# Kernel optimization log

Hardware: AMD Instinct MI355X
Metric: run time of the kernel (lower is better)

Reference implementation:

```python
import jax, jax.numpy as jnp
import numpy as np

N = 8192
E = 131072
D_IN = 128
D_OUT = 128
EPS = 1e-5


def setup_inputs() -> dict:
    key = jax.random.key(0)
    k1, k2, k3, k4 = jax.random.split(key, 4)
    x = jax.random.normal(k1, (N, D_IN), dtype=jnp.float32)
    edge_index = jax.random.randint(k2, (2, E), 0, N, dtype=jnp.int64)
    weight = jax.random.normal(k3, (D_IN, D_OUT), dtype=jnp.float32)
    bias = jax.random.normal(k4, (D_OUT,), dtype=jnp.float32)
    return {"x": x, "edge_index": edge_index, "weight": weight, "bias": bias}


def reference(x, edge_index, weight, bias):
    n = x.shape[0]
    row, col = edge_index[0], edge_index[1]
    # dense adjacency build, exactly as the torch module does
    adj = jnp.zeros((n, n), dtype=x.dtype).at[row, col].set(1.0)
    adj = jnp.maximum(adj, adj.T)                      # symmetrize
    adj = adj + jnp.eye(n, dtype=x.dtype)              # self-loops (added, may yield 2 on diag)
    d_inv_sqrt = 1.0 / jnp.sqrt(adj.sum(axis=1) + EPS)  # [N]
    # D^{-1/2} A D^{-1/2} via broadcasting (same math as diag matmuls)
    norm_adj = d_inv_sqrt[:, None] * adj * d_inv_sqrt[None, :]
    out = norm_adj @ x            # [N, D_IN] aggregation
    out = out @ weight + bias     # [N, D_OUT]
    return out
```

## Files before the change

### kernel.cpp

```cpp
#include <hip/hip_runtime.h>
#include <stdint.h>

#define N_NODES 8192
#define NE      131072
#define DCH     128
#define WPR     256
#define MAXC    128
#define EPS     1e-5f

__global__ __launch_bounds__(256) void build_gemm_kernel(
    const void*  __restrict__ ei_raw,
    const float* __restrict__ X,
    const float* __restrict__ W,
    uint32_t* __restrict__ bm,
    int*      __restrict__ deg,
    float*    __restrict__ z)
{
    int t = threadIdx.x;
    if (blockIdx.x < 512) {
        int lane = t & 63;
        const long long* p64 = (const long long*)ei_raw;
        const int*       p32 = (const int*)ei_raw;
        bool is64 = __all((unsigned long long)p64[lane] < (unsigned long long)N_NODES);
        int e = blockIdx.x * 256 + t;
        int r, c;
        if (is64) { r = (int)p64[e]; c = (int)p64[NE + e]; }
        else      { r = p32[e];      c = p32[NE + e]; }
        uint32_t mc = 1u << (c & 31), mr = 1u << (r & 31);
        uint32_t o1 = atomicOr(&bm[r * WPR + (c >> 5)], mc);
        if (!(o1 & mc)) atomicAdd(&deg[r], 1);
        uint32_t o2 = atomicOr(&bm[c * WPR + (r >> 5)], mr);
        if (!(o2 & mr)) atomicAdd(&deg[c], 1);
    } else {
        __shared__ float sA[64][132];
        int bx = blockIdx.x - 512;
        int row0 = (bx >> 1) * 64;
        int col0 = (bx & 1) * 64;
        {
            int k4 = t & 31;
            int r  = t >> 5;
            #pragma unroll
            for (int p = 0; p < 8; ++p) {
                float4 v = *(const float4*)&X[(size_t)(row0 + r + p * 8) * DCH + k4 * 4];
                *(float4*)&sA[r + p * 8][k4 * 4] = v;
            }
        }
        __syncthreads();
        int tx = t & 15, ty = t >> 4;
        int cg = col0 + tx * 4;
        int r0 = ty * 4;
        float acc[4][4] = {};
        #pragma unroll 4
        for (int k = 0; k < DCH; ++k) {
            float4 w = *(const float4*)&W[(size_t)k * DCH + cg];
            float a0 = sA[r0 + 0][k];
            float a1 = sA[r0 + 1][k];
            float a2 = sA[r0 + 2][k];
            float a3 = sA[r0 + 3][k];
            acc[0][0] += a0 * w.x; acc[0][1] += a0 * w.y; acc[0][2] += a0 * w.z; acc[0][3] += a0 * w.w;
            acc[1][0] += a1 * w.x; acc[1][1] += a1 * w.y; acc[1][2] += a1 * w.z; acc[1][3] += a1 * w.w;
            acc[2][0] += a2 * w.x; acc[2][1] += a2 * w.y; acc[2][2] += a2 * w.z; acc[2][3] += a2 * w.w;
            acc[3][0] += a3 * w.x; acc[3][1] += a3 * w.y; acc[3][2] += a3 * w.z; acc[3][3] += a3 * w.w;
        }
        #pragma unroll
        for (int i = 0; i < 4; ++i) {
            float4 o;
            o.x = acc[i][0]; o.y = acc[i][1]; o.z = acc[i][2]; o.w = acc[i][3];
            *(float4*)&z[(size_t)(row0 + r0 + i) * DCH + cg] = o;
        }
    }
}

__global__ __launch_bounds__(256) void aggregate_kernel(
    const uint4* __restrict__ bm4,
    const int*   __restrict__ deg,
    const float* __restrict__ z,
    const float* __restrict__ bias,
    float*       __restrict__ out)
{
    __shared__ uint16_t slist[4][MAXC];
    int w    = threadIdx.x >> 6;
    int lane = threadIdx.x & 63;
    int node = blockIdx.x * 4 + w;

    uint4 b = bm4[(size_t)node * 64 + lane];
    int c = __popc(b.x) + __popc(b.y) + __popc(b.z) + __popc(b.w);
    int pre = c;
    #pragma unroll
    for (int d = 1; d < 64; d <<= 1) {
        int v = __shfl_up(pre, d);
        if (lane >= d) pre += v;
    }
    int total = __shfl(pre, 63);
    int excl  = pre - c;

    {
        uint32_t wd[4] = {b.x, b.y, b.z, b.w};
        int basebit = lane * 128;
        int o = excl;
        #pragma unroll
        for (int m = 0; m < 4; ++m) {
            uint32_t v = wd[m];
            while (v) {
                int bb = __ffs(v) - 1; v &= v - 1;
                if (o < MAXC) slist[w][o] = (uint16_t)(basebit + m * 32 + bb);
                ++o;
            }
        }
    }
    int cap  = total > MAXC ? MAXC : total;
    int kpad = (cap + 7) & ~7;
    int p = cap + lane;
    if (p < kpad) slist[w][p] = (uint16_t)node;

    const float2* z2 = (const float2*)z;
    float dn = 1.0f / sqrtf((float)total + 1.0f + EPS);

    float2 self = z2[(size_t)node * 64 + lane];
    float2 a0, a1 = {0,0}, a2 = {0,0}, a3 = {0,0}, a4 = {0,0}, a5 = {0,0}, a6 = {0,0}, a7 = {0,0};
    a0.x = dn * self.x; a0.y = dn * self.y;

    for (int k = 0; k < kpad; k += 8) {
        #define STEP(i, AX) {                                                        \
            int idx = k + i;                                                         \
            int j = __builtin_amdgcn_readfirstlane((int)slist[w][idx]);              \
            float dj = (idx < cap) ? 1.0f / sqrtf((float)deg[j] + 1.0f + EPS) : 0.f; \
            float2 q = z2[(size_t)j * 64 + lane];                                    \
            AX.x += dj * q.x; AX.y += dj * q.y; }
        STEP(0, a0) STEP(1, a1) STEP(2, a2) STEP(3, a3)
        STEP(4, a4) STEP(5, a5) STEP(6, a6) STEP(7, a7)
        #undef STEP
    }

    float2 bb = ((const float2*)bias)[lane];
    float2 r;
    r.x = dn * (((a0.x + a1.x) + (a2.x + a3.x)) + ((a4.x + a5.x) + (a6.x + a7.x))) + bb.x;
    r.y = dn * (((a0.y + a1.y) + (a2.y + a3.y)) + ((a4.y + a5.y) + (a6.y + a7.y))) + bb.y;
    ((float2*)out)[(size_t)node * 64 + lane] = r;
}

extern "C" void kernel_launch(void* const* d_in, const int* in_sizes, int n_in,
                              void* d_out, int out_size, void* d_ws, size_t ws_size,
                              hipStream_t stream) {
    const float* xp  = (const float*)d_in[0];
    const void*  eip = d_in[1];
    const float* Wp  = (const float*)d_in[2];
    const float* bp  = (const float*)d_in[3];
    float*       op  = (float*)d_out;

    uint8_t* ws = (uint8_t*)d_ws;
    uint32_t* bmp  = (uint32_t*)ws;
    int*      degp = (int*)     (ws + (size_t)8 * 1024 * 1024);
    float*    zp   = (float*)   (ws + (size_t)8 * 1024 * 1024 + 32 * 1024);

    hipMemsetAsync(bmp, 0, (size_t)8 * 1024 * 1024 + 32 * 1024, stream);
    build_gemm_kernel<<<768, 256, 0, stream>>>(eip, xp, Wp, bmp, degp, zp);
    aggregate_kernel<<<N_NODES / 4, 256, 0, stream>>>((const uint4*)bmp, degp, zp, bp, op);
}
```

Before: 118.4 us.

## Build per-node neighbor lists during edge scatter instead of scanning bitmaps

The edge-scatter stage now appends each newly seen neighbor into a per-node uint16 list of up to 128 entries, reserving the slot with the atomic counter. The aggregation kernel reads that compact list, 256 bytes per node, instead of scanning the 1 KB bitmap row with popcounts, a prefix scan and bit extraction. The padded tail iterations are also split out of the main loop so the main loop needs no validity checks. Neighbor order now follows atomic arrival order, so the float summation order becomes nondeterministic. The list buffer is not cleared by the memset, but only entries below the count are read.

```diff
diff --git a/kernel.cpp b/kernel.cpp
--- a/kernel.cpp
+++ b/kernel.cpp
@@ -13,7 +13,8 @@
     const float* __restrict__ X,
     const float* __restrict__ W,
     uint32_t* __restrict__ bm,
-    int*      __restrict__ deg,
+    int*      __restrict__ cnt,
+    uint16_t* __restrict__ nbr,
     float*    __restrict__ z)
 {
     int t = threadIdx.x;
@@ -28,9 +29,15 @@
         else      { r = p32[e];      c = p32[NE + e]; }
         uint32_t mc = 1u << (c & 31), mr = 1u << (r & 31);
         uint32_t o1 = atomicOr(&bm[r * WPR + (c >> 5)], mc);
-        if (!(o1 & mc)) atomicAdd(&deg[r], 1);
+        if (!(o1 & mc)) {
+            int pos = atomicAdd(&cnt[r], 1);
+            if (pos < MAXC) nbr[(size_t)r * MAXC + pos] = (uint16_t)c;
+        }
         uint32_t o2 = atomicOr(&bm[c * WPR + (r >> 5)], mr);
-        if (!(o2 & mr)) atomicAdd(&deg[c], 1);
+        if (!(o2 & mr)) {
+            int pos = atomicAdd(&cnt[c], 1);
+            if (pos < MAXC) nbr[(size_t)c * MAXC + pos] = (uint16_t)r;
+        }
     } else {
         __shared__ float sA[64][132];
         int bx = blockIdx.x - 512;
@@ -72,64 +79,52 @@
 }
 
 __global__ __launch_bounds__(256) void aggregate_kernel(
-    const uint4* __restrict__ bm4,
-    const int*   __restrict__ deg,
+    const uint16_t* __restrict__ nbr,
+    const int*   __restrict__ cnt,
     const float* __restrict__ z,
     const float* __restrict__ bias,
     float*       __restrict__ out)
 {
-    __shared__ uint16_t slist[4][MAXC];
+    __shared__ uint32_t s_list[4][64];
     int w    = threadIdx.x >> 6;
     int lane = threadIdx.x & 63;
     int node = blockIdx.x * 4 + w;
 
-    uint4 b = bm4[(size_t)node * 64 + lane];
-    int c = __popc(b.x) + __popc(b.y) + __popc(b.z) + __popc(b.w);
-    int pre = c;
-    #pragma unroll
-    for (int d = 1; d < 64; d <<= 1) {
-        int v = __shfl_up(pre, d);
-        if (lane >= d) pre += v;
-    }
-    int total = __shfl(pre, 63);
-    int excl  = pre - c;
+    s_list[w][lane] = ((const uint32_t*)nbr)[(size_t)node * (MAXC / 2) + lane];
+    const uint16_t* sl = (const uint16_t*)s_list[w];
 
-    {
-        uint32_t wd[4] = {b.x, b.y, b.z, b.w};
-        int basebit = lane * 128;
-        int o = excl;
-        #pragma unroll
-        for (int m = 0; m < 4; ++m) {
-            uint32_t v = wd[m];
-            while (v) {
-                int bb = __ffs(v) - 1; v &= v - 1;
-                if (o < MAXC) slist[w][o] = (uint16_t)(basebit + m * 32 + bb);
-                ++o;
-            }
-        }
-    }
-    int cap  = total > MAXC ? MAXC : total;
-    int kpad = (cap + 7) & ~7;
-    int p = cap + lane;
-    if (p < kpad) slist[w][p] = (uint16_t)node;
+    int total = __builtin_amdgcn_readfirstlane(cnt[node]);
+    int cap   = total > MAXC ? MAXC : total;
+    int full  = cap & ~7;
+    float dn  = 1.0f / sqrtf((float)total + 1.0f + EPS);
 
     const float2* z2 = (const float2*)z;
-    float dn = 1.0f / sqrtf((float)total + 1.0f + EPS);
-
     float2 self = z2[(size_t)node * 64 + lane];
     float2 a0, a1 = {0,0}, a2 = {0,0}, a3 = {0,0}, a4 = {0,0}, a5 = {0,0}, a6 = {0,0}, a7 = {0,0};
     a0.x = dn * self.x; a0.y = dn * self.y;
 
-    for (int k = 0; k < kpad; k += 8) {
-        #define STEP(i, AX) {                                                        \
-            int idx = k + i;                                                         \
-            int j = __builtin_amdgcn_readfirstlane((int)slist[w][idx]);              \
-            float dj = (idx < cap) ? 1.0f / sqrtf((float)deg[j] + 1.0f + EPS) : 0.f; \
-            float2 q = z2[(size_t)j * 64 + lane];                                    \
+    for (int k = 0; k < full; k += 8) {
+        #define STEPU(i, AX) {                                                \
+            int j = __builtin_amdgcn_readfirstlane((int)sl[k + i]);           \
+            float dj = 1.0f / sqrtf((float)cnt[j] + 1.0f + EPS);              \
+            float2 q = z2[(size_t)j * 64 + lane];                             \
             AX.x += dj * q.x; AX.y += dj * q.y; }
-        STEP(0, a0) STEP(1, a1) STEP(2, a2) STEP(3, a3)
-        STEP(4, a4) STEP(5, a5) STEP(6, a6) STEP(7, a7)
-        #undef STEP
+        STEPU(0, a0) STEPU(1, a1) STEPU(2, a2) STEPU(3, a3)
+        STEPU(4, a4) STEPU(5, a5) STEPU(6, a6) STEPU(7, a7)
+        #undef STEPU
+    }
+    if (full < cap) {
+        #define STEPP(i, AX) {                                                \
+            int idx = full + i;                                               \
+            int j = __builtin_amdgcn_readfirstlane((int)sl[idx]);             \
+            bool val = idx < cap;                                             \
+            j = val ? j : node;                                               \
+            float dj = val ? 1.0f / sqrtf((float)cnt[j] + 1.0f + EPS) : 0.0f; \
+            float2 q = z2[(size_t)j * 64 + lane];                             \
+            AX.x += dj * q.x; AX.y += dj * q.y; }
+        STEPP(0, a0) STEPP(1, a1) STEPP(2, a2) STEPP(3, a3)
+        STEPP(4, a4) STEPP(5, a5) STEPP(6, a6) STEPP(7, a7)
+        #undef STEPP
     }
 
     float2 bb = ((const float2*)bias)[lane];
@@ -150,10 +145,11 @@
 
     uint8_t* ws = (uint8_t*)d_ws;
     uint32_t* bmp  = (uint32_t*)ws;
-    int*      degp = (int*)     (ws + (size_t)8 * 1024 * 1024);
-    float*    zp   = (float*)   (ws + (size_t)8 * 1024 * 1024 + 32 * 1024);
+    int*      cntp = (int*)     (ws + (size_t)8 * 1024 * 1024);
+    uint16_t* nbrp = (uint16_t*)(ws + (size_t)8 * 1024 * 1024 + 32 * 1024);
+    float*    zp   = (float*)   (ws + (size_t)10 * 1024 * 1024 + 32 * 1024);
 
     hipMemsetAsync(bmp, 0, (size_t)8 * 1024 * 1024 + 32 * 1024, stream);
-    build_gemm_kernel<<<768, 256, 0, stream>>>(eip, xp, Wp, bmp, degp, zp);
-    aggregate_kernel<<<N_NODES / 4, 256, 0, stream>>>((const uint4*)bmp, degp, zp, bp, op);
+    build_gemm_kernel<<<768, 256, 0, stream>>>(eip, xp, Wp, bmp, cntp, nbrp, zp);
+    aggregate_kernel<<<N_NODES / 4, 256, 0, stream>>>(nbrp, cntp, zp, bp, op);
 }
```

New measurement: 119.3 us. No clear change (+0.8%).
